# Optimization experiments

Hardware: AMD Instinct MI355X
Metric: run time of the kernel (lower is better)

Reference implementation:

```python
import jax, jax.numpy as jnp
import numpy as np

N_NODES = 100000
IN_CH = 128
OUT_CH = 128
N_EDGES = 1600000
BN_EPS = 1e-5


def setup_inputs() -> dict:
    key = jax.random.key(0)
    ks = jax.random.split(key, 8)
    x = jax.random.normal(ks[0], (N_NODES, IN_CH), dtype=jnp.float32)
    edge_index = jax.random.randint(ks[1], (2, N_EDGES), 0, N_NODES, dtype=jnp.int64)
    # xavier_uniform for Linear weights, zero bias (matches reset_parameters)
    lim1 = float(np.sqrt(6.0 / (IN_CH + OUT_CH)))
    W1 = jax.random.uniform(ks[2], (OUT_CH, IN_CH), minval=-lim1, maxval=lim1, dtype=jnp.float32)
    b1 = jnp.zeros((OUT_CH,), jnp.float32)
    lim2 = float(np.sqrt(6.0 / (OUT_CH + OUT_CH)))
    W2 = jax.random.uniform(ks[3], (OUT_CH, OUT_CH), minval=-lim2, maxval=lim2, dtype=jnp.float32)
    b2 = jnp.zeros((OUT_CH,), jnp.float32)
    gamma = jnp.ones((OUT_CH,), jnp.float32)
    beta = jnp.zeros((OUT_CH,), jnp.float32)
    eps = jnp.zeros((1,), jnp.float32)  # GIN epsilon parameter (init 0.0)
    return {"x": x, "edge_index": edge_index, "eps": eps,
            "W1": W1, "b1": b1, "gamma": gamma, "beta": beta,
            "W2": W2, "b2": b2}


def reference(x, edge_index, eps, W1, b1, gamma, beta, W2, b2):
    row, col = edge_index[0], edge_index[1]
    # gather source features and scatter-add into destination nodes
    aggr = jax.ops.segment_sum(x[row], col, num_segments=x.shape[0])  # [N, C]
    out = (1.0 + eps) * x + aggr
    # MLP: Linear -> BatchNorm1d (batch stats, training mode) -> ReLU -> Linear
    h = out @ W1.T + b1
    mean = jnp.mean(h, axis=0)
    var = jnp.var(h, axis=0)  # biased, as BatchNorm normalization uses
    h = (h - mean) * jax.lax.rsqrt(var + BN_EPS) * gamma + beta
    h = jax.nn.relu(h)
    return h @ W2.T + b2
```

## Files before the change

### kernel.cpp

```cpp
#include <hip/hip_runtime.h>


constexpr int   NNODES = 100000;
constexpr int   CH     = 128;
constexpr long  NE     = 1600000;
constexpr float BN_EPS = 1e-5f;
constexpr int   SCAN_B = 1024;
constexpr int   NSCAN  = (NNODES + SCAN_B - 1) / SCAN_B;

__global__ __launch_bounds__(256) void k_hist(const int* __restrict__ ei,
                                              int* __restrict__ offsets) {
  long e = (long)blockIdx.x * blockDim.x + threadIdx.x;
  if (e >= NE) return;
  atomicAdd(&offsets[1 + ei[NE + e]], 1);
}

__global__ __launch_bounds__(SCAN_B) void k_scan1(int* __restrict__ offsets,
                                                  int* __restrict__ partials) {
  __shared__ int sm[SCAN_B];
  const int t = threadIdx.x;
  const long idx = (long)blockIdx.x * SCAN_B + t;
  int v = (idx < NNODES) ? offsets[1 + idx] : 0;
  sm[t] = v;
  __syncthreads();
  for (int off = 1; off < SCAN_B; off <<= 1) {
    int u = (t >= off) ? sm[t - off] : 0;
    __syncthreads();
    sm[t] += u;
    __syncthreads();
  }
  if (idx < NNODES) offsets[1 + idx] = sm[t];
  if (t == SCAN_B - 1) partials[blockIdx.x] = sm[t];
}

__global__ void k_scan2(int* __restrict__ partials, int* __restrict__ pexcl) {
  if (threadIdx.x == 0) {
    int run = 0;
    for (int b = 0; b < NSCAN; ++b) { pexcl[b] = run; run += partials[b]; }
  }
}

__global__ __launch_bounds__(SCAN_B) void k_scan3(int* __restrict__ offsets,
                                                  const int* __restrict__ pexcl,
                                                  int* __restrict__ cursor) {
  const long idx = (long)blockIdx.x * SCAN_B + threadIdx.x;
  if (idx < NNODES) offsets[1 + idx] += pexcl[blockIdx.x];
}

__global__ __launch_bounds__(256) void k_curinit(const int* __restrict__ offsets,
                                                 int* __restrict__ cursor) {
  const long idx = (long)blockIdx.x * blockDim.x + threadIdx.x;
  if (idx < NNODES) cursor[idx] = offsets[idx];
}

__global__ __launch_bounds__(256) void k_fill(const int* __restrict__ ei,
                                              int* __restrict__ cursor,
                                              int* __restrict__ srcs) {
  long e = (long)blockIdx.x * blockDim.x + threadIdx.x;
  if (e >= NE) return;
  const int src = ei[e];
  const int dst = ei[NE + e];
  const int p = atomicAdd(&cursor[dst], 1);
  srcs[p] = src;
}

__global__ __launch_bounds__(256) void k_aggr(const float* __restrict__ x,
                                              const float* __restrict__ eps,
                                              const int* __restrict__ offsets,
                                              const int* __restrict__ srcs,
                                              float* __restrict__ out) {
  const int n = blockIdx.x * 4 + (threadIdx.x >> 6);
  if (n >= NNODES) return;
  const int lane = threadIdx.x & 63;
  const int beg = offsets[n];
  const int end = offsets[n + 1];
  float2 acc = make_float2(0.f, 0.f);
  for (int p = beg; p < end; ++p) {
    const int s = srcs[p];
    const float2 v = *reinterpret_cast<const float2*>(x + (long)s * CH + lane * 2);
    acc.x += v.x; acc.y += v.y;
  }
  const float sc = 1.0f + eps[0];
  const float2 xv = *reinterpret_cast<const float2*>(x + (long)n * CH + lane * 2);
  float2 o;
  o.x = fmaf(xv.x, sc, acc.x);
  o.y = fmaf(xv.y, sc, acc.y);
  *reinterpret_cast<float2*>(out + (long)n * CH + lane * 2) = o;
}

template <bool BN>
__global__ __launch_bounds__(256) void k_gemm(const float* __restrict__ A,
                                              const float* __restrict__ W,
                                              const float* __restrict__ bias,
                                              const float* __restrict__ stats,
                                              float* __restrict__ Cout) {
  __shared__ float xs[64][132];
  __shared__ float wsT[32][132];
  const int tid  = threadIdx.x;
  const int row0 = blockIdx.x * 64;
  const int nrows = min(64, NNODES - row0);

  for (int l = 0; l < 8; ++l) {
    const int fi = l * 256 + tid;
    const int r  = fi >> 5;
    const int kq = fi & 31;
    float4 v = make_float4(0.f, 0.f, 0.f, 0.f);
    if (r < nrows)
      v = *reinterpret_cast<const float4*>(A + (long)(row0 + r) * CH + kq * 4);
    if (BN) {
      const int k = kq * 4;
      v.x = fmaxf(fmaf(v.x, stats[256 + k + 0], stats[384 + k + 0]), 0.f);
      v.y = fmaxf(fmaf(v.y, stats[256 + k + 1], stats[384 + k + 1]), 0.f);
      v.z = fmaxf(fmaf(v.z, stats[256 + k + 2], stats[384 + k + 2]), 0.f);
      v.w = fmaxf(fmaf(v.w, stats[256 + k + 3], stats[384 + k + 3]), 0.f);
    }
    *reinterpret_cast<float4*>(&xs[r][kq * 4]) = v;
  }

  float acc[4][8];
#pragma unroll
  for (int i = 0; i < 4; ++i)
#pragma unroll
    for (int j = 0; j < 8; ++j) acc[i][j] = 0.f;

  const int tc = tid & 15;
  const int tr = tid >> 4;
  const int r0 = tr * 4;
  const int c0 = tc * 8;

  for (int kb = 0; kb < 128; kb += 32) {
    __syncthreads();
#pragma unroll
    for (int l = 0; l < 16; ++l) {
      const int idx = l * 256 + tid;
      const int c   = idx >> 5;
      const int kk  = idx & 31;
      wsT[kk][c] = W[c * CH + kb + kk];
    }
    __syncthreads();
#pragma unroll
    for (int kk = 0; kk < 32; ++kk) {
      const float4 w0 = *reinterpret_cast<const float4*>(&wsT[kk][c0]);
      const float4 w1 = *reinterpret_cast<const float4*>(&wsT[kk][c0 + 4]);
      float xr[4];
#pragma unroll
      for (int i = 0; i < 4; ++i) xr[i] = xs[r0 + i][kb + kk];
#pragma unroll
      for (int i = 0; i < 4; ++i) {
        acc[i][0] = fmaf(xr[i], w0.x, acc[i][0]);
        acc[i][1] = fmaf(xr[i], w0.y, acc[i][1]);
        acc[i][2] = fmaf(xr[i], w0.z, acc[i][2]);
        acc[i][3] = fmaf(xr[i], w0.w, acc[i][3]);
        acc[i][4] = fmaf(xr[i], w1.x, acc[i][4]);
        acc[i][5] = fmaf(xr[i], w1.y, acc[i][5]);
        acc[i][6] = fmaf(xr[i], w1.z, acc[i][6]);
        acc[i][7] = fmaf(xr[i], w1.w, acc[i][7]);
      }
    }
  }

  const float4 bv0 = *reinterpret_cast<const float4*>(bias + c0);
  const float4 bv1 = *reinterpret_cast<const float4*>(bias + c0 + 4);
#pragma unroll
  for (int i = 0; i < 4; ++i) {
    const int r = r0 + i;
    if (r < nrows) {
      float4 o0, o1;
      o0.x = acc[i][0] + bv0.x; o0.y = acc[i][1] + bv0.y;
      o0.z = acc[i][2] + bv0.z; o0.w = acc[i][3] + bv0.w;
      o1.x = acc[i][4] + bv1.x; o1.y = acc[i][5] + bv1.y;
      o1.z = acc[i][6] + bv1.z; o1.w = acc[i][7] + bv1.w;
      float* p = Cout + (long)(row0 + r) * CH + c0;
      *reinterpret_cast<float4*>(p)     = o0;
      *reinterpret_cast<float4*>(p + 4) = o1;
    }
  }
}

__global__ __launch_bounds__(128) void k_stats(const float* __restrict__ h,
                                               float* __restrict__ stats,
                                               int rows_per_block) {
  const int c = threadIdx.x;
  long r0 = (long)blockIdx.x * rows_per_block;
  long r1 = min((long)NNODES, r0 + rows_per_block);
  float s = 0.f, s2 = 0.f;
  for (long r = r0; r < r1; ++r) {
    const float v = h[r * CH + c];
    s += v;
    s2 = fmaf(v, v, s2);
  }
  atomicAdd(&stats[c], s);
  atomicAdd(&stats[CH + c], s2);
}

__global__ __launch_bounds__(128) void k_finalize(float* __restrict__ stats,
                                                  const float* __restrict__ gamma,
                                                  const float* __restrict__ beta) {
  const int c = threadIdx.x;
  const float inv_n = 1.0f / (float)NNODES;
  const float mean = stats[c] * inv_n;
  const float var  = stats[CH + c] * inv_n - mean * mean;
  const float sc   = gamma[c] * rsqrtf(var + BN_EPS);
  stats[256 + c] = sc;
  stats[384 + c] = beta[c] - mean * sc;
}

extern "C" void kernel_launch(void* const* d_in, const int* in_sizes, int n_in,
                              void* d_out, int out_size, void* d_ws, size_t ws_size,
                              hipStream_t stream) {
  const float* x     = (const float*)d_in[0];
  const int*   ei    = (const int*)d_in[1];
  const float* eps   = (const float*)d_in[2];
  const float* W1    = (const float*)d_in[3];
  const float* b1    = (const float*)d_in[4];
  const float* gamma = (const float*)d_in[5];
  const float* beta  = (const float*)d_in[6];
  const float* W2    = (const float*)d_in[7];
  const float* b2    = (const float*)d_in[8];
  float* out = (float*)d_out;

  int* offsets   = (int*)d_ws;
  int* cursor    = offsets + (NNODES + 1);
  int* srcs      = cursor + NNODES;
  float* stats   = (float*)(srcs + NE);
  int* partials  = (int*)(stats + 512);
  int* pexcl     = partials + NSCAN;

  hipMemsetAsync(offsets, 0, (NNODES + 1) * sizeof(int), stream);
  hipMemsetAsync(stats, 0, 256 * sizeof(float), stream);

  const int eblk = (int)((NE + 255) / 256);
  k_hist<<<eblk, 256, 0, stream>>>(ei, offsets);
  k_scan1<<<NSCAN, SCAN_B, 0, stream>>>(offsets, partials);
  k_scan2<<<1, 64, 0, stream>>>(partials, pexcl);
  k_scan3<<<NSCAN, SCAN_B, 0, stream>>>(offsets, pexcl, cursor);
  k_curinit<<<(NNODES + 255) / 256, 256, 0, stream>>>(offsets, cursor);
  k_fill<<<eblk, 256, 0, stream>>>(ei, cursor, srcs);

  k_aggr<<<(NNODES + 3) / 4, 256, 0, stream>>>(x, eps, offsets, srcs, out);

  k_gemm<false><<<(NNODES + 63) / 64, 256, 0, stream>>>(out, W1, b1, nullptr, out);

  const int nblk = 1024;
  const int rpb = (NNODES + nblk - 1) / nblk;
  k_stats<<<nblk, 128, 0, stream>>>(out, stats, rpb);
  k_finalize<<<1, 128, 0, stream>>>(stats, gamma, beta);

  k_gemm<true><<<(NNODES + 63) / 64, 256, 0, stream>>>(out, W2, b2, stats, out);
}
```

Before: 667.7 us.

## Gather neighbor features from a bf16 copy of x and fuse scan/cursor kernels

Adds a kernel that converts x to bf16 once per call, and the aggregation gathers 4-byte packed bf16 pairs instead of float2. This halves the bytes read in the random-access neighbor gather. Separately, the scan stages are merged: each block sums the preceding partials itself, and cursor initialization is folded into the offset-fixup kernel, which removes two launches. The cost is bf16 rounding of neighbor features, which lowers accuracy, plus an extra conversion pass over x.

After: 597.7 us. 1.12x faster.

```diff
diff --git a/kernel.cpp b/kernel.cpp
--- a/kernel.cpp
+++ b/kernel.cpp
@@ -7,6 +7,23 @@
 constexpr float BN_EPS = 1e-5f;
 constexpr int   SCAN_B = 1024;
 constexpr int   NSCAN  = (NNODES + SCAN_B - 1) / SCAN_B;
+
+__device__ __forceinline__ unsigned short f2b(float f) {
+  unsigned int u = __float_as_uint(f);
+  unsigned int r = (u + 0x7fffu + ((u >> 16) & 1u)) >> 16;
+  return (unsigned short)r;
+}
+
+__global__ __launch_bounds__(256) void k_x2b(const float* __restrict__ x,
+                                             unsigned short* __restrict__ xb) {
+  long i = (long)blockIdx.x * 256 + threadIdx.x;
+  const long n4 = (long)NNODES * CH / 4;
+  if (i >= n4) return;
+  float4 v = reinterpret_cast<const float4*>(x)[i];
+  ushort4 o;
+  o.x = f2b(v.x); o.y = f2b(v.y); o.z = f2b(v.z); o.w = f2b(v.w);
+  reinterpret_cast<ushort4*>(xb)[i] = o;
+}
 
 __global__ __launch_bounds__(256) void k_hist(const int* __restrict__ ei,
                                               int* __restrict__ offsets) {
@@ -33,24 +50,23 @@
   if (t == SCAN_B - 1) partials[blockIdx.x] = sm[t];
 }
 
-__global__ void k_scan2(int* __restrict__ partials, int* __restrict__ pexcl) {
+__global__ __launch_bounds__(SCAN_B) void k_scan3(int* __restrict__ offsets,
+                                                  const int* __restrict__ partials,
+                                                  int* __restrict__ cursor) {
+  __shared__ int base_sm;
   if (threadIdx.x == 0) {
     int run = 0;
-    for (int b = 0; b < NSCAN; ++b) { pexcl[b] = run; run += partials[b]; }
-  }
-}
-
-__global__ __launch_bounds__(SCAN_B) void k_scan3(int* __restrict__ offsets,
-                                                  const int* __restrict__ pexcl,
-                                                  int* __restrict__ cursor) {
+    for (int b = 0; b < blockIdx.x; ++b) run += partials[b];
+    base_sm = run;
+  }
+  __syncthreads();
   const long idx = (long)blockIdx.x * SCAN_B + threadIdx.x;
-  if (idx < NNODES) offsets[1 + idx] += pexcl[blockIdx.x];
-}
-
-__global__ __launch_bounds__(256) void k_curinit(const int* __restrict__ offsets,
-                                                 int* __restrict__ cursor) {
-  const long idx = (long)blockIdx.x * blockDim.x + threadIdx.x;
-  if (idx < NNODES) cursor[idx] = offsets[idx];
+  if (idx < NNODES) {
+    const int v = offsets[1 + idx] + base_sm;
+    offsets[1 + idx] = v;
+    if (idx == 0) cursor[0] = 0;
+    if (idx < NNODES - 1) cursor[idx + 1] = v;
+  }
 }
 
 __global__ __launch_bounds__(256) void k_fill(const int* __restrict__ ei,
@@ -65,6 +81,7 @@
 }
 
 __global__ __launch_bounds__(256) void k_aggr(const float* __restrict__ x,
+                                              const unsigned int* __restrict__ xb32,
                                               const float* __restrict__ eps,
                                               const int* __restrict__ offsets,
                                               const int* __restrict__ srcs,
@@ -74,17 +91,19 @@
   const int lane = threadIdx.x & 63;
   const int beg = offsets[n];
   const int end = offsets[n + 1];
-  float2 acc = make_float2(0.f, 0.f);
+  float ax = 0.f, ay = 0.f;
+#pragma unroll 4
   for (int p = beg; p < end; ++p) {
     const int s = srcs[p];
-    const float2 v = *reinterpret_cast<const float2*>(x + (long)s * CH + lane * 2);
-    acc.x += v.x; acc.y += v.y;
+    const unsigned int u = xb32[(long)s * 64 + lane];
+    ax += __uint_as_float(u << 16);
+    ay += __uint_as_float(u & 0xffff0000u);
   }
   const float sc = 1.0f + eps[0];
   const float2 xv = *reinterpret_cast<const float2*>(x + (long)n * CH + lane * 2);
   float2 o;
-  o.x = fmaf(xv.x, sc, acc.x);
-  o.y = fmaf(xv.y, sc, acc.y);
+  o.x = fmaf(xv.x, sc, ax);
+  o.y = fmaf(xv.y, sc, ay);
   *reinterpret_cast<float2*>(out + (long)n * CH + lane * 2) = o;
 }
 
@@ -224,20 +243,22 @@
   int* srcs      = cursor + NNODES;
   float* stats   = (float*)(srcs + NE);
   int* partials  = (int*)(stats + 512);
-  int* pexcl     = partials + NSCAN;
+  unsigned short* xb = (unsigned short*)(partials + NSCAN);
 
   hipMemsetAsync(offsets, 0, (NNODES + 1) * sizeof(int), stream);
   hipMemsetAsync(stats, 0, 256 * sizeof(float), stream);
+
+  const long n4 = (long)NNODES * CH / 4;
+  k_x2b<<<(int)((n4 + 255) / 256), 256, 0, stream>>>(x, xb);
 
   const int eblk = (int)((NE + 255) / 256);
   k_hist<<<eblk, 256, 0, stream>>>(ei, offsets);
   k_scan1<<<NSCAN, SCAN_B, 0, stream>>>(offsets, partials);
-  k_scan2<<<1, 64, 0, stream>>>(partials, pexcl);
-  k_scan3<<<NSCAN, SCAN_B, 0, stream>>>(offsets, pexcl, cursor);
-  k_curinit<<<(NNODES + 255) / 256, 256, 0, stream>>>(offsets, cursor);
+  k_scan3<<<NSCAN, SCAN_B, 0, stream>>>(offsets, partials, cursor);
   k_fill<<<eblk, 256, 0, stream>>>(ei, cursor, srcs);
 
-  k_aggr<<<(NNODES + 3) / 4, 256, 0, stream>>>(x, eps, offsets, srcs, out);
+  k_aggr<<<(NNODES + 3) / 4, 256, 0, stream>>>(
+      x, (const unsigned int*)xb, eps, offsets, srcs, out);
 
   k_gemm<false><<<(NNODES + 63) / 64, 256, 0, stream>>>(out, W1, b1, nullptr, out);
 
```
